# Kernel tuning notes

Measured on AMD Instinct MI355X. Metric: run time of the kernel, lower is better.

## Reference

```python
import jax, jax.numpy as jnp
import numpy as np

CAPACITY_FACTOR = 1.25


def setup_inputs() -> dict:
    key = jax.random.key(0)
    ks = jax.random.split(key, 5)
    B, N, D, E, H = 4, 2048, 1024, 8, 4096
    x = jax.random.normal(ks[0], (B, N, D), dtype=jnp.float32)
    w_router = jax.random.normal(ks[1], (D, E), dtype=jnp.float32) * 0.02
    w1 = jax.random.normal(ks[2], (E, D, H), dtype=jnp.float32) * 0.02
    b1 = jnp.zeros((E, H), dtype=jnp.float32)
    w2 = jax.random.normal(ks[3], (E, H, D), dtype=jnp.float32) * 0.02
    b2 = jnp.zeros((E, D), dtype=jnp.float32)
    return {"x": x, "w_router": w_router, "w1": w1, "b1": b1, "w2": w2, "b2": b2}


def reference(x, w_router, w1, b1, w2, b2):
    B, N, D = x.shape
    E = w_router.shape[1]
    C = int(N * CAPACITY_FACTOR // E)  # expert capacity

    # ---- top-1 switch router ----
    logits = jnp.einsum('bnd,de->bne', x, w_router)                 # [B,N,E]
    z = jax.nn.logsumexp(logits, axis=-1)                           # [B,N]
    router_z_loss = jnp.mean(z * z)
    probs = jax.nn.softmax(logits, axis=-1)                         # [B,N,E]
    gate = jnp.max(probs, axis=-1)                                  # [B,N]
    idx = jnp.argmax(probs, axis=-1)                                # [B,N]
    mask = jax.nn.one_hot(idx, E, dtype=x.dtype)                    # [B,N,E]

    # load-balancing aux loss (Switch-Transformer style)
    density = jnp.mean(mask, axis=1)                                # [B,E] fraction routed
    density_proxy = jnp.mean(probs, axis=1)                         # [B,E] mean router prob
    aux_loss = jnp.mean(jnp.sum(density * density_proxy, axis=-1)) * (E * E)

    # position within each expert; drop tokens beyond capacity
    pos = jnp.cumsum(mask, axis=1) - 1.0                            # [B,N,E]
    pos = pos.astype(jnp.int32)
    # one_hot zeros out indices outside [0,C); mask zeros unrouted slots
    dispatch = mask[..., None] * jax.nn.one_hot(pos, C, dtype=x.dtype)  # [B,N,E,C]
    combine = dispatch * gate[:, :, None, None]                     # [B,N,E,C]

    # ---- dense dispatch -> grouped expert FFN -> dense combine ----
    expert_inputs = jnp.einsum('bnd,bnec->becd', x, dispatch)       # [B,E,C,D]
    h = jax.nn.gelu(jnp.einsum('becd,edh->bech', expert_inputs, w1)
                    + b1[None, :, None, :])                          # [B,E,C,H]
    expert_outputs = jnp.einsum('bech,ehd->becd', h, w2) + b2[None, :, None, :]
    output = jnp.einsum('becd,bnec->bnd', expert_outputs, combine)  # [B,N,D]
    return output, aux_loss, router_z_loss
```

## Files before the change

kernel.cpp:

```cpp
#include <hip/hip_runtime.h>
#include <hip/hip_bf16.h>
#include <math.h>

#define B_ 4
#define N_ 2048
#define D_ 1024
#define E_ 8
#define H_ 4096
#define C_ 320
#define M_ (B_*C_)

typedef __attribute__((ext_vector_type(8))) short short8;
typedef __attribute__((ext_vector_type(4))) float floatx4;

__device__ __forceinline__ unsigned short f2bf(float f) {
  unsigned u = __builtin_bit_cast(unsigned, f);
  u += 0x7fffu + ((u >> 16) & 1u);
  return (unsigned short)(u >> 16);
}

__device__ __forceinline__ float gelu_fast(float x) {
  float u = 0.7978845608028654f * (x + 0.044715f * x * x * x);
  float t = 1.f - 2.f / (__expf(2.f * u) + 1.f);
  return 0.5f * x * (1.f + t);
}

__device__ __forceinline__ void gload_lds16(const unsigned short* g, unsigned short* l) {
  __builtin_amdgcn_global_load_lds(
      (const __attribute__((address_space(1))) unsigned int*)g,
      (__attribute__((address_space(3))) unsigned int*)l, 16, 0, 0);
}

__global__ __launch_bounds__(256) void router_kernel(
    const float* __restrict__ x, const float* __restrict__ wr,
    int* __restrict__ idx_buf, float* __restrict__ gate_buf,
    float* __restrict__ stats)
{
  int lane  = threadIdx.x & 63;
  int wave  = threadIdx.x >> 6;
  int token = blockIdx.x * 4 + wave;
  int b     = token >> 11;

  const float* xp = x + (size_t)token * D_ + lane * 16;
  float xv[16];
#pragma unroll
  for (int i = 0; i < 4; i++) {
    float4 v = ((const float4*)xp)[i];
    xv[i*4+0]=v.x; xv[i*4+1]=v.y; xv[i*4+2]=v.z; xv[i*4+3]=v.w;
  }
  double acc[8];
#pragma unroll
  for (int e = 0; e < 8; e++) acc[e] = 0.0;
  const float* wp = wr + (size_t)(lane * 16) * E_;
#pragma unroll
  for (int i = 0; i < 16; i++) {
    float xs = xv[i];
#pragma unroll
    for (int e = 0; e < 8; e++) acc[e] += (double)xs * (double)wp[i*8 + e];
  }
  for (int off = 32; off > 0; off >>= 1) {
#pragma unroll
    for (int e = 0; e < 8; e++) acc[e] += __shfl_xor(acc[e], off, 64);
  }

  float l[8];
#pragma unroll
  for (int e = 0; e < 8; e++) l[e] = (float)acc[e];
  float m = l[0]; int best = 0;
#pragma unroll
  for (int e = 1; e < 8; e++) if (l[e] > m) { m = l[e]; best = e; }
  float p[8], sum = 0.f;
#pragma unroll
  for (int e = 0; e < 8; e++) { p[e] = expf(l[e] - m); sum += p[e]; }
  float inv = 1.f / sum;
#pragma unroll
  for (int e = 0; e < 8; e++) p[e] *= inv;
  float z    = m + logf(sum);
  float gate = inv;

  __shared__ float s_cnt[8], s_prox[8], s_zsq[1];
  if (threadIdx.x < 8)  { s_cnt[threadIdx.x] = 0.f; s_prox[threadIdx.x] = 0.f; }
  if (threadIdx.x == 8) s_zsq[0] = 0.f;
  __syncthreads();
  if (lane == 0) {
    idx_buf[token]  = best;
    gate_buf[token] = gate;
    atomicAdd(&s_zsq[0], z * z);
    atomicAdd(&s_cnt[best], 1.f);
#pragma unroll
    for (int e = 0; e < 8; e++) atomicAdd(&s_prox[e], p[e]);
  }
  __syncthreads();
  if (threadIdx.x < 8) {
    atomicAdd(&stats[b*8 + threadIdx.x],      s_cnt[threadIdx.x]);
    atomicAdd(&stats[32 + b*8 + threadIdx.x], s_prox[threadIdx.x]);
  }
  if (threadIdx.x == 8) atomicAdd(&stats[64], s_zsq[0]);
}

__global__ __launch_bounds__(64) void pos_kernel(
    const int* __restrict__ idx_buf, int* __restrict__ slot_token,
    const float* __restrict__ stats, float* __restrict__ loss_out)
{
  int be = blockIdx.x;
  int b = be >> 3, e = be & 7;
  int lane = threadIdx.x;
  int base = 0;
  int* out = slot_token + (size_t)(e * B_ + b) * C_;
  for (int n0 = 0; n0 < N_; n0 += 64) {
    int n = n0 + lane;
    bool match = (idx_buf[b * N_ + n] == e);
    unsigned long long mask = __ballot(match);
    int my = base + __popcll(mask & ((1ull << lane) - 1ull));
    if (match && my < C_) out[my] = b * N_ + n;
    base += __popcll(mask);
  }
  if (be == 0 && lane == 0) {
    float aux = 0.f;
    for (int i = 0; i < 32; i++) aux += stats[i] * stats[32 + i];
    aux *= 64.f / ((float)B_ * (float)N_ * (float)N_);
    loss_out[0] = aux;
    loss_out[1] = stats[64] / (float)(B_ * N_);
  }
}

__global__ __launch_bounds__(256) void gather_kernel(
    const float* __restrict__ x, const int* __restrict__ slot_token,
    unsigned short* __restrict__ xe)
{
  int row = blockIdx.x;
  int t = slot_token[row];
  int col = threadIdx.x * 4;
  ushort4 o;
  if (t >= 0) {
    float4 v = *(const float4*)(x + (size_t)t * D_ + col);
    o.x = f2bf(v.x); o.y = f2bf(v.y); o.z = f2bf(v.z); o.w = f2bf(v.w);
  } else {
    o.x = 0; o.y = 0; o.z = 0; o.w = 0;
  }
  *(ushort4*)(xe + (size_t)row * D_ + col) = o;
}

__global__ __launch_bounds__(256) void transcast_kernel(
    const float* __restrict__ in, unsigned short* __restrict__ out, int R, int Cc)
{
  int e = blockIdx.z;
  const float* pin = in + (size_t)e * R * Cc;
  unsigned short* pout = out + (size_t)e * R * Cc;
  __shared__ float T[64][65];
  int r0 = blockIdx.y * 64, c0 = blockIdx.x * 64;
  {
    int row = threadIdx.x >> 2;
    int cb  = (threadIdx.x & 3) * 4;
#pragma unroll
    for (int p = 0; p < 4; p++) {
      int col = cb + p * 16;
      float4 v = *(const float4*)(pin + (size_t)(r0 + row) * Cc + c0 + col);
      T[row][col+0] = v.x; T[row][col+1] = v.y; T[row][col+2] = v.z; T[row][col+3] = v.w;
    }
  }
  __syncthreads();
  {
    int ocb = threadIdx.x >> 4;
    int or4 = (threadIdx.x & 15) * 4;
#pragma unroll
    for (int p = 0; p < 4; p++) {
      int oc = ocb + p * 16;
      ushort4 o;
      o.x = f2bf(T[or4+0][oc]); o.y = f2bf(T[or4+1][oc]);
      o.z = f2bf(T[or4+2][oc]); o.w = f2bf(T[or4+3][oc]);
      *(ushort4*)(pout + (size_t)(c0 + oc) * R + r0 + or4) = o;
    }
  }
}

template<int EPI>
__global__ __launch_bounds__(256) void gemm_kernel(
    const unsigned short* __restrict__ A,
    const unsigned short* __restrict__ BT,
    const float* __restrict__ bias,
    unsigned short* __restrict__ Hout,
    float* __restrict__ Out,
    const int* __restrict__ slot_token,
    const float* __restrict__ gate_buf,
    int M, int K, int Nn, int MT)
{
  int e  = blockIdx.x & 7;
  int s  = blockIdx.x >> 3;
  int m0 = (s % MT) * 128;
  int n0 = (s / MT) * 128;
  const unsigned short* Ae = A  + (size_t)e * M  * K;
  const unsigned short* Be = BT + (size_t)e * Nn * K;

  __shared__ __align__(16) unsigned short As[2][128 * 32];
  __shared__ __align__(16) unsigned short Bs[2][128 * 32];
  __shared__ int   s_tok[128];
  __shared__ float s_gate[128];

  int tid  = threadIdx.x;
  int lane = tid & 63;
  int wave = tid >> 6;
  int wm   = (wave >> 1) * 64;
  int wn   = (wave & 1) * 64;
  int lr   = lane & 15;
  int quad = lane >> 4;

  if constexpr (EPI == 1) {
    if (tid < 128) {
      int t = slot_token[(size_t)e * M + m0 + tid];
      s_tok[tid]  = t;
      s_gate[tid] = (t >= 0) ? gate_buf[t] : 0.f;
    }
  }

  floatx4 acc[4][4];
#pragma unroll
  for (int i = 0; i < 4; i++)
#pragma unroll
    for (int j = 0; j < 4; j++) acc[i][j] = (floatx4){0.f, 0.f, 0.f, 0.f};

  int rA0 = wave * 32 + (lane >> 2);
  int kcc = (lane & 3) * 8;
  const unsigned short* Ag0 = Ae + (size_t)(m0 + rA0)      * K + kcc;
  const unsigned short* Ag1 = Ae + (size_t)(m0 + rA0 + 16) * K + kcc;
  const unsigned short* Bg0 = Be + (size_t)(n0 + rA0)      * K + kcc;
  const unsigned short* Bg1 = Be + (size_t)(n0 + rA0 + 16) * K + kcc;
  const unsigned offA0 = (wave * 32) * 32;
  const unsigned offA1 = (wave * 32 + 16) * 32;

  gload_lds16(Ag0, &As[0][offA0]);
  gload_lds16(Ag1, &As[0][offA1]);
  gload_lds16(Bg0, &Bs[0][offA0]);
  gload_lds16(Bg1, &Bs[0][offA1]);
  Ag0 += 32; Ag1 += 32; Bg0 += 32; Bg1 += 32;

  int nIter = K >> 5;
  int buf = 0;
  for (int it = 0; it < nIter; ++it) {
    __syncthreads();
    if (it + 1 < nIter) {
      gload_lds16(Ag0, &As[buf ^ 1][offA0]);
      gload_lds16(Ag1, &As[buf ^ 1][offA1]);
      gload_lds16(Bg0, &Bs[buf ^ 1][offA0]);
      gload_lds16(Bg1, &Bs[buf ^ 1][offA1]);
      Ag0 += 32; Ag1 += 32; Bg0 += 32; Bg1 += 32;
    }
    short8 af[4], bf[4];
#pragma unroll
    for (int i = 0; i < 4; i++) {
      af[i] = *(const short8*)(&As[buf][(wm + i * 16 + lr) * 32 + quad * 8]);
      bf[i] = *(const short8*)(&Bs[buf][(wn + i * 16 + lr) * 32 + quad * 8]);
    }
#pragma unroll
    for (int i = 0; i < 4; i++)
#pragma unroll
      for (int j = 0; j < 4; j++)
        acc[i][j] = __builtin_amdgcn_mfma_f32_16x16x32_bf16(af[i], bf[j], acc[i][j], 0, 0, 0);
    buf ^= 1;
  }

#pragma unroll
  for (int i = 0; i < 4; i++) {
    int rloc = wm + i * 16 + quad * 4;
#pragma unroll
    for (int j = 0; j < 4; j++) {
      int col = n0 + wn + j * 16 + lr;
      float bz = bias[(size_t)e * Nn + col];
      if constexpr (EPI == 0) {
        size_t base = (size_t)e * M * Nn + (size_t)(m0 + rloc) * Nn + col;
#pragma unroll
        for (int r = 0; r < 4; r++)
          Hout[base + (size_t)r * Nn] = f2bf(gelu_fast(acc[i][j][r] + bz));
      } else {
#pragma unroll
        for (int r = 0; r < 4; r++) {
          int t = s_tok[rloc + r];
          if (t >= 0)
            Out[(size_t)t * D_ + col] = s_gate[rloc + r] * (acc[i][j][r] + bz);
        }
      }
    }
  }
}

extern "C" void kernel_launch(void* const* d_in, const int* in_sizes, int n_in,
                              void* d_out, int out_size, void* d_ws, size_t ws_size,
                              hipStream_t stream)
{
  (void)in_sizes; (void)n_in; (void)ws_size;
  const float* x  = (const float*)d_in[0];
  const float* wr = (const float*)d_in[1];
  const float* w1 = (const float*)d_in[2];
  const float* b1 = (const float*)d_in[3];
  const float* w2 = (const float*)d_in[4];
  const float* b2 = (const float*)d_in[5];
  float* out = (float*)d_out;

  char* ws = (char*)d_ws;
  int*   idx_buf  = (int*)(ws + 0);
  float* gate_buf = (float*)(ws + 32768);
  float* stats    = (float*)(ws + 65536);
  int*   slot_tok = (int*)(ws + 66560);
  unsigned short* xe  = (unsigned short*)(ws + 107520);
  unsigned short* wbf = (unsigned short*)(ws + 21079040);
  unsigned short* hbf = (unsigned short*)(ws + 88187904);

  hipMemsetAsync(d_out, 0, (size_t)out_size * 4, stream);
  hipMemsetAsync(stats, 0, 1024, stream);
  hipMemsetAsync(slot_tok, 0xFF, (size_t)E_ * B_ * C_ * 4, stream);

  router_kernel<<<(B_ * N_) / 4, 256, 0, stream>>>(x, wr, idx_buf, gate_buf, stats);
  pos_kernel<<<B_ * E_, 64, 0, stream>>>(idx_buf, slot_tok, stats,
                                         out + (size_t)B_ * N_ * D_);
  gather_kernel<<<E_ * M_, 256, 0, stream>>>(x, slot_tok, xe);

  transcast_kernel<<<dim3(H_ / 64, D_ / 64, E_), 256, 0, stream>>>(w1, wbf, D_, H_);
  gemm_kernel<0><<<E_ * (H_ / 128) * (M_ / 128), 256, 0, stream>>>(
      xe, wbf, b1, hbf, nullptr, nullptr, nullptr, M_, D_, H_, M_ / 128);
  transcast_kernel<<<dim3(D_ / 64, H_ / 64, E_), 256, 0, stream>>>(w2, wbf, H_, D_);
  gemm_kernel<1><<<E_ * (D_ / 128) * (M_ / 128), 256, 0, stream>>>(
      hbf, wbf, b2, nullptr, out, slot_tok, gate_buf, M_, H_, D_, M_ / 128);
}
```

Baseline: 644.6 us.

## Enlarge expert GEMM tiles to 256x256x64 with swizzled LDS and interleaved prefetch

The grouped expert GEMMs move from 128x128 tiles with K-step 32 and 4 waves to 256x256 tiles with K-step 64 and 8 waves. Each wave now computes a 128x64 sub-tile, and the LDS layout uses an XOR swizzle to avoid bank conflicts. The main loop is split into four MFMA phases, with explicit barriers, wave-priority hints and staged global-to-LDS prefetches of the next A and B slices. The aim is more data reuse per load and better overlap of loads with MFMA work. The trade-off is 128KB of LDS per block, which allows only one block per CU, and far fewer blocks: the second GEMM gets only 160 blocks, which may leave many of the GPU's CUs idle.

```diff
diff --git a/kernel.cpp b/kernel.cpp
--- a/kernel.cpp
+++ b/kernel.cpp
@@ -175,7 +175,7 @@
 }
 
 template<int EPI>
-__global__ __launch_bounds__(256) void gemm_kernel(
+__global__ __launch_bounds__(512, 2) void gemm_kernel(
     const unsigned short* __restrict__ A,
     const unsigned short* __restrict__ BT,
     const float* __restrict__ bias,
@@ -187,96 +187,188 @@
 {
   int e  = blockIdx.x & 7;
   int s  = blockIdx.x >> 3;
-  int m0 = (s % MT) * 128;
-  int n0 = (s / MT) * 128;
+  int m0 = (s % MT) * 256;
+  int n0 = (s / MT) * 256;
   const unsigned short* Ae = A  + (size_t)e * M  * K;
   const unsigned short* Be = BT + (size_t)e * Nn * K;
 
-  __shared__ __align__(16) unsigned short As[2][128 * 32];
-  __shared__ __align__(16) unsigned short Bs[2][128 * 32];
-  __shared__ int   s_tok[128];
-  __shared__ float s_gate[128];
+  __shared__ __align__(16) unsigned short As[2][256 * 64];
+  __shared__ __align__(16) unsigned short Bs[2][256 * 64];
+  __shared__ int   s_tok[256];
+  __shared__ float s_gate[256];
 
   int tid  = threadIdx.x;
   int lane = tid & 63;
-  int wave = tid >> 6;
-  int wm   = (wave >> 1) * 64;
-  int wn   = (wave & 1) * 64;
+  int w    = tid >> 6;
+  int wm   = (w >> 2) * 128;
+  int wn   = (w & 3) * 64;
   int lr   = lane & 15;
   int quad = lane >> 4;
+  int c0 = (((quad    ) ^ (lane & 7)) << 3);
+  int c1 = (((quad + 4) ^ (lane & 7)) << 3);
 
   if constexpr (EPI == 1) {
-    if (tid < 128) {
+    if (tid < 256) {
       int t = slot_token[(size_t)e * M + m0 + tid];
       s_tok[tid]  = t;
       s_gate[tid] = (t >= 0) ? gate_buf[t] : 0.f;
     }
   }
 
-  floatx4 acc[4][4];
-#pragma unroll
-  for (int i = 0; i < 4; i++)
+  floatx4 acc[8][4];
+#pragma unroll
+  for (int i = 0; i < 8; i++)
 #pragma unroll
     for (int j = 0; j < 4; j++) acc[i][j] = (floatx4){0.f, 0.f, 0.f, 0.f};
 
-  int rA0 = wave * 32 + (lane >> 2);
-  int kcc = (lane & 3) * 8;
-  const unsigned short* Ag0 = Ae + (size_t)(m0 + rA0)      * K + kcc;
-  const unsigned short* Ag1 = Ae + (size_t)(m0 + rA0 + 16) * K + kcc;
-  const unsigned short* Bg0 = Be + (size_t)(n0 + rA0)      * K + kcc;
-  const unsigned short* Bg1 = Be + (size_t)(n0 + rA0 + 16) * K + kcc;
-  const unsigned offA0 = (wave * 32) * 32;
-  const unsigned offA1 = (wave * 32 + 16) * 32;
-
-  gload_lds16(Ag0, &As[0][offA0]);
-  gload_lds16(Ag1, &As[0][offA1]);
-  gload_lds16(Bg0, &Bs[0][offA0]);
-  gload_lds16(Bg1, &Bs[0][offA1]);
-  Ag0 += 32; Ag1 += 32; Bg0 += 32; Bg1 += 32;
-
-  int nIter = K >> 5;
-  int buf = 0;
-  for (int it = 0; it < nIter; ++it) {
-    __syncthreads();
-    if (it + 1 < nIter) {
-      gload_lds16(Ag0, &As[buf ^ 1][offA0]);
-      gload_lds16(Ag1, &As[buf ^ 1][offA1]);
-      gload_lds16(Bg0, &Bs[buf ^ 1][offA0]);
-      gload_lds16(Bg1, &Bs[buf ^ 1][offA1]);
-      Ag0 += 32; Ag1 += 32; Bg0 += 32; Bg1 += 32;
-    }
-    short8 af[4], bf[4];
-#pragma unroll
-    for (int i = 0; i < 4; i++) {
-      af[i] = *(const short8*)(&As[buf][(wm + i * 16 + lr) * 32 + quad * 8]);
-      bf[i] = *(const short8*)(&Bs[buf][(wn + i * 16 + lr) * 32 + quad * 8]);
-    }
-#pragma unroll
-    for (int i = 0; i < 4; i++)
-#pragma unroll
-      for (int j = 0; j < 4; j++)
-        acc[i][j] = __builtin_amdgcn_mfma_f32_16x16x32_bf16(af[i], bf[j], acc[i][j], 0, 0, 0);
-    buf ^= 1;
-  }
-
-#pragma unroll
-  for (int i = 0; i < 4; i++) {
-    int rloc = wm + i * 16 + quad * 4;
-#pragma unroll
-    for (int j = 0; j < 4; j++) {
-      int col = n0 + wn + j * 16 + lr;
+  int rrow = lane >> 3;
+  int sch  = ((lane & 7) ^ rrow) << 3;
+  const unsigned short* gA00 = Ae + (size_t)(m0       + w*16     + rrow) * K + sch;
+  const unsigned short* gA01 = Ae + (size_t)(m0       + w*16 + 8 + rrow) * K + sch;
+  const unsigned short* gA10 = Ae + (size_t)(m0 + 128 + w*16     + rrow) * K + sch;
+  const unsigned short* gA11 = Ae + (size_t)(m0 + 128 + w*16 + 8 + rrow) * K + sch;
+  const unsigned short* gB00 = Be + (size_t)(n0       + w*16     + rrow) * K + sch;
+  const unsigned short* gB01 = Be + (size_t)(n0       + w*16 + 8 + rrow) * K + sch;
+  const unsigned short* gB10 = Be + (size_t)(n0 + 128 + w*16     + rrow) * K + sch;
+  const unsigned short* gB11 = Be + (size_t)(n0 + 128 + w*16 + 8 + rrow) * K + sch;
+
+#define STAGE_A0(dbuf) do { \
+    gload_lds16(gA00, &As[dbuf][(w*16    ) * 64]); \
+    gload_lds16(gA01, &As[dbuf][(w*16 + 8) * 64]); \
+    gA00 += 64; gA01 += 64; } while (0)
+#define STAGE_A1(dbuf) do { \
+    gload_lds16(gA10, &As[dbuf][(128 + w*16    ) * 64]); \
+    gload_lds16(gA11, &As[dbuf][(128 + w*16 + 8) * 64]); \
+    gA10 += 64; gA11 += 64; } while (0)
+#define STAGE_B0(dbuf) do { \
+    gload_lds16(gB00, &Bs[dbuf][(w*16    ) * 64]); \
+    gload_lds16(gB01, &Bs[dbuf][(w*16 + 8) * 64]); \
+    gB00 += 64; gB01 += 64; } while (0)
+#define STAGE_B1(dbuf) do { \
+    gload_lds16(gB10, &Bs[dbuf][(128 + w*16    ) * 64]); \
+    gload_lds16(gB11, &Bs[dbuf][(128 + w*16 + 8) * 64]); \
+    gB10 += 64; gB11 += 64; } while (0)
+
+  int nt = K >> 6;
+  STAGE_A0(0); STAGE_A1(0); STAGE_B0(0); STAGE_B1(0);
+  if (nt > 1) {
+    STAGE_A0(1); STAGE_A1(1);
+    asm volatile("s_waitcnt vmcnt(4)" ::: "memory");
+  } else {
+    asm volatile("s_waitcnt vmcnt(0)" ::: "memory");
+  }
+  __builtin_amdgcn_s_barrier();
+
+  short8 af[4][2], bf[4][2];
+  int cur = 0;
+  for (int t = 0; t < nt; ++t) {
+    int nxt = cur ^ 1;
+#pragma unroll
+    for (int m = 0; m < 4; ++m) {
+      int row = wm + m * 16 + lr;
+      af[m][0] = *(const short8*)&As[cur][row * 64 + c0];
+      af[m][1] = *(const short8*)&As[cur][row * 64 + c1];
+    }
+#pragma unroll
+    for (int n = 0; n < 2; ++n) {
+      int row = wn + n * 16 + lr;
+      bf[n][0] = *(const short8*)&Bs[cur][row * 64 + c0];
+      bf[n][1] = *(const short8*)&Bs[cur][row * 64 + c1];
+    }
+    if (t + 1 < nt) STAGE_B0(nxt);
+    __builtin_amdgcn_s_barrier();
+    asm volatile("s_waitcnt lgkmcnt(0)" ::: "memory");
+    __builtin_amdgcn_sched_barrier(0);
+    __builtin_amdgcn_s_setprio(1);
+#pragma unroll
+    for (int m = 0; m < 4; ++m)
+#pragma unroll
+      for (int n = 0; n < 2; ++n) {
+        acc[m][n] = __builtin_amdgcn_mfma_f32_16x16x32_bf16(af[m][0], bf[n][0], acc[m][n], 0, 0, 0);
+        acc[m][n] = __builtin_amdgcn_mfma_f32_16x16x32_bf16(af[m][1], bf[n][1], acc[m][n], 0, 0, 0);
+      }
+    __builtin_amdgcn_s_setprio(0);
+    __builtin_amdgcn_s_barrier();
+#pragma unroll
+    for (int n = 0; n < 2; ++n) {
+      int row = wn + (n + 2) * 16 + lr;
+      bf[n+2][0] = *(const short8*)&Bs[cur][row * 64 + c0];
+      bf[n+2][1] = *(const short8*)&Bs[cur][row * 64 + c1];
+    }
+    if (t + 1 < nt) STAGE_B1(nxt);
+    __builtin_amdgcn_s_barrier();
+    asm volatile("s_waitcnt lgkmcnt(0)" ::: "memory");
+    __builtin_amdgcn_sched_barrier(0);
+    __builtin_amdgcn_s_setprio(1);
+#pragma unroll
+    for (int m = 0; m < 4; ++m)
+#pragma unroll
+      for (int n = 2; n < 4; ++n) {
+        acc[m][n] = __builtin_amdgcn_mfma_f32_16x16x32_bf16(af[m][0], bf[n][0], acc[m][n], 0, 0, 0);
+        acc[m][n] = __builtin_amdgcn_mfma_f32_16x16x32_bf16(af[m][1], bf[n][1], acc[m][n], 0, 0, 0);
+      }
+    __builtin_amdgcn_s_setprio(0);
+    __builtin_amdgcn_s_barrier();
+#pragma unroll
+    for (int m = 0; m < 4; ++m) {
+      int row = wm + 64 + m * 16 + lr;
+      af[m][0] = *(const short8*)&As[cur][row * 64 + c0];
+      af[m][1] = *(const short8*)&As[cur][row * 64 + c1];
+    }
+    __builtin_amdgcn_s_barrier();
+    asm volatile("s_waitcnt lgkmcnt(0)" ::: "memory");
+    __builtin_amdgcn_sched_barrier(0);
+    __builtin_amdgcn_s_setprio(1);
+#pragma unroll
+    for (int m = 0; m < 4; ++m)
+#pragma unroll
+      for (int n = 2; n < 4; ++n) {
+        acc[m+4][n] = __builtin_amdgcn_mfma_f32_16x16x32_bf16(af[m][0], bf[n][0], acc[m+4][n], 0, 0, 0);
+        acc[m+4][n] = __builtin_amdgcn_mfma_f32_16x16x32_bf16(af[m][1], bf[n][1], acc[m+4][n], 0, 0, 0);
+      }
+    __builtin_amdgcn_s_setprio(0);
+    __builtin_amdgcn_s_barrier();
+    if (t + 2 < nt) { STAGE_A0(cur); STAGE_A1(cur); }
+    __builtin_amdgcn_s_barrier();
+    __builtin_amdgcn_s_setprio(1);
+#pragma unroll
+    for (int m = 0; m < 4; ++m)
+#pragma unroll
+      for (int n = 0; n < 2; ++n) {
+        acc[m+4][n] = __builtin_amdgcn_mfma_f32_16x16x32_bf16(af[m][0], bf[n][0], acc[m+4][n], 0, 0, 0);
+        acc[m+4][n] = __builtin_amdgcn_mfma_f32_16x16x32_bf16(af[m][1], bf[n][1], acc[m+4][n], 0, 0, 0);
+      }
+    __builtin_amdgcn_s_setprio(0);
+    if (t + 1 < nt) {
+      if (t + 2 < nt) asm volatile("s_waitcnt vmcnt(4)" ::: "memory");
+      else            asm volatile("s_waitcnt vmcnt(0)" ::: "memory");
+    }
+    __builtin_amdgcn_s_barrier();
+    cur = nxt;
+  }
+#undef STAGE_A0
+#undef STAGE_A1
+#undef STAGE_B0
+#undef STAGE_B1
+
+#pragma unroll
+  for (int m = 0; m < 8; ++m) {
+    int rloc = wm + m * 16 + quad * 4;
+#pragma unroll
+    for (int n = 0; n < 4; ++n) {
+      int col = n0 + wn + n * 16 + lr;
       float bz = bias[(size_t)e * Nn + col];
       if constexpr (EPI == 0) {
         size_t base = (size_t)e * M * Nn + (size_t)(m0 + rloc) * Nn + col;
 #pragma unroll
         for (int r = 0; r < 4; r++)
-          Hout[base + (size_t)r * Nn] = f2bf(gelu_fast(acc[i][j][r] + bz));
+          Hout[base + (size_t)r * Nn] = f2bf(gelu_fast(acc[m][n][r] + bz));
       } else {
 #pragma unroll
         for (int r = 0; r < 4; r++) {
           int t = s_tok[rloc + r];
           if (t >= 0)
-            Out[(size_t)t * D_ + col] = s_gate[rloc + r] * (acc[i][j][r] + bz);
+            Out[(size_t)t * D_ + col] = s_gate[rloc + r] * (acc[m][n][r] + bz);
         }
       }
     }
@@ -315,9 +407,9 @@
   gather_kernel<<<E_ * M_, 256, 0, stream>>>(x, slot_tok, xe);
 
   transcast_kernel<<<dim3(H_ / 64, D_ / 64, E_), 256, 0, stream>>>(w1, wbf, D_, H_);
-  gemm_kernel<0><<<E_ * (H_ / 128) * (M_ / 128), 256, 0, stream>>>(
-      xe, wbf, b1, hbf, nullptr, nullptr, nullptr, M_, D_, H_, M_ / 128);
+  gemm_kernel<0><<<E_ * (H_ / 256) * (M_ / 256), 512, 0, stream>>>(
+      xe, wbf, b1, hbf, nullptr, nullptr, nullptr, M_, D_, H_, M_ / 256);
   transcast_kernel<<<dim3(D_ / 64, H_ / 64, E_), 256, 0, stream>>>(w2, wbf, H_, D_);
-  gemm_kernel<1><<<E_ * (D_ / 128) * (M_ / 128), 256, 0, stream>>>(
-      hbf, wbf, b2, nullptr, out, slot_tok, gate_buf, M_, H_, D_, M_ / 128);
-}
+  gemm_kernel<1><<<E_ * (D_ / 256) * (M_ / 256), 512, 0, stream>>>(
+      hbf, wbf, b2, nullptr, out, slot_tok, gate_buf, M_, H_, D_, M_ / 256);
+}
```

Measured after the change: 665.3 us. 3.2% more time.

## Swizzle LDS tiles, add explicit waitcnt/barrier pipeline and occupancy hint in GEMM

Applied to the files above, without the earlier changes.

Rewrites the GEMM main loop so global-to-LDS loads use an XOR-swizzled column chunk, and the fragment reads apply the matching swizzle. The goal is to avoid LDS bank conflicts on the short8 reads. The plain __syncthreads is replaced with explicit vmcnt/lgkmcnt waits, raw s_barrier, sched_barrier and setprio around the MFMA block, and launch_bounds now requests 4 blocks per CU. The intent is better overlap and less stalling, at the risk of register pressure under the occupancy cap and a full vmcnt(0) wait each iteration.

```diff
diff --git a/kernel.cpp b/kernel.cpp
--- a/kernel.cpp
+++ b/kernel.cpp
@@ -175,7 +175,7 @@
 }
 
 template<int EPI>
-__global__ __launch_bounds__(256) void gemm_kernel(
+__global__ __launch_bounds__(256, 4) void gemm_kernel(
     const unsigned short* __restrict__ A,
     const unsigned short* __restrict__ BT,
     const float* __restrict__ bias,
@@ -199,11 +199,12 @@
 
   int tid  = threadIdx.x;
   int lane = tid & 63;
-  int wave = tid >> 6;
-  int wm   = (wave >> 1) * 64;
-  int wn   = (wave & 1) * 64;
+  int w    = tid >> 6;
+  int wm   = (w >> 1) * 64;
+  int wn   = (w & 1) * 64;
   int lr   = lane & 15;
   int quad = lane >> 4;
+  int rch  = ((quad ^ ((lr >> 1) & 3)) << 3);
 
   if constexpr (EPI == 1) {
     if (tid < 128) {
@@ -219,64 +220,71 @@
 #pragma unroll
     for (int j = 0; j < 4; j++) acc[i][j] = (floatx4){0.f, 0.f, 0.f, 0.f};
 
-  int rA0 = wave * 32 + (lane >> 2);
-  int kcc = (lane & 3) * 8;
-  const unsigned short* Ag0 = Ae + (size_t)(m0 + rA0)      * K + kcc;
-  const unsigned short* Ag1 = Ae + (size_t)(m0 + rA0 + 16) * K + kcc;
-  const unsigned short* Bg0 = Be + (size_t)(n0 + rA0)      * K + kcc;
-  const unsigned short* Bg1 = Be + (size_t)(n0 + rA0 + 16) * K + kcc;
-  const unsigned offA0 = (wave * 32) * 32;
-  const unsigned offA1 = (wave * 32 + 16) * 32;
-
-  gload_lds16(Ag0, &As[0][offA0]);
-  gload_lds16(Ag1, &As[0][offA1]);
-  gload_lds16(Bg0, &Bs[0][offA0]);
-  gload_lds16(Bg1, &Bs[0][offA1]);
-  Ag0 += 32; Ag1 += 32; Bg0 += 32; Bg1 += 32;
-
-  int nIter = K >> 5;
-  int buf = 0;
-  for (int it = 0; it < nIter; ++it) {
-    __syncthreads();
-    if (it + 1 < nIter) {
-      gload_lds16(Ag0, &As[buf ^ 1][offA0]);
-      gload_lds16(Ag1, &As[buf ^ 1][offA1]);
-      gload_lds16(Bg0, &Bs[buf ^ 1][offA0]);
-      gload_lds16(Bg1, &Bs[buf ^ 1][offA1]);
-      Ag0 += 32; Ag1 += 32; Bg0 += 32; Bg1 += 32;
-    }
-    short8 af[4], bf[4];
-#pragma unroll
-    for (int i = 0; i < 4; i++) {
-      af[i] = *(const short8*)(&As[buf][(wm + i * 16 + lr) * 32 + quad * 8]);
-      bf[i] = *(const short8*)(&Bs[buf][(wn + i * 16 + lr) * 32 + quad * 8]);
-    }
-#pragma unroll
-    for (int i = 0; i < 4; i++)
-#pragma unroll
-      for (int j = 0; j < 4; j++)
-        acc[i][j] = __builtin_amdgcn_mfma_f32_16x16x32_bf16(af[i], bf[j], acc[i][j], 0, 0, 0);
-    buf ^= 1;
-  }
-
-#pragma unroll
-  for (int i = 0; i < 4; i++) {
-    int rloc = wm + i * 16 + quad * 4;
-#pragma unroll
-    for (int j = 0; j < 4; j++) {
-      int col = n0 + wn + j * 16 + lr;
+  unsigned kA   = (unsigned)K * 2;
+  unsigned soff = (unsigned)((lane & 3) ^ ((lane >> 3) & 3)) * 16u
+                + (unsigned)(lane >> 2) * kA;
+  unsigned aoff = (unsigned)(m0 + w * 16) * kA + soff;
+  unsigned boff = (unsigned)(n0 + w * 16) * kA + soff;
+  const char* AeC = (const char*)Ae;
+  const char* BeC = (const char*)Be;
+
+#define STAGE_A(dbuf) do { \
+    gload_lds16((const unsigned short*)(AeC + aoff),           &As[dbuf][(w * 16) * 32]); \
+    gload_lds16((const unsigned short*)(AeC + aoff + 64 * kA), &As[dbuf][(64 + w * 16) * 32]); \
+    aoff += 64; } while (0)
+#define STAGE_B(dbuf) do { \
+    gload_lds16((const unsigned short*)(BeC + boff),           &Bs[dbuf][(w * 16) * 32]); \
+    gload_lds16((const unsigned short*)(BeC + boff + 64 * kA), &Bs[dbuf][(64 + w * 16) * 32]); \
+    boff += 64; } while (0)
+
+  int nt = K >> 5;
+  STAGE_A(0); STAGE_B(0);
+  asm volatile("s_waitcnt vmcnt(0)" ::: "memory");
+  __builtin_amdgcn_s_barrier();
+
+  for (int t = 0; t < nt; ++t) {
+    int cur = t & 1, nxt = cur ^ 1;
+    if (t + 1 < nt) { STAGE_A(nxt); STAGE_B(nxt); }
+    short8 a[4], b[4];
+#pragma unroll
+    for (int m = 0; m < 4; ++m)
+      a[m] = *(const short8*)&As[cur][(wm + m * 16 + lr) * 32 + rch];
+#pragma unroll
+    for (int n = 0; n < 4; ++n)
+      b[n] = *(const short8*)&Bs[cur][(wn + n * 16 + lr) * 32 + rch];
+    asm volatile("s_waitcnt lgkmcnt(0)" ::: "memory");
+    __builtin_amdgcn_sched_barrier(0);
+    __builtin_amdgcn_s_setprio(1);
+#pragma unroll
+    for (int m = 0; m < 4; ++m)
+#pragma unroll
+      for (int n = 0; n < 4; ++n)
+        acc[m][n] = __builtin_amdgcn_mfma_f32_16x16x32_bf16(a[m], b[n], acc[m][n], 0, 0, 0);
+    __builtin_amdgcn_s_setprio(0);
+    if (t + 1 < nt) asm volatile("s_waitcnt vmcnt(0)" ::: "memory");
+    __builtin_amdgcn_s_barrier();
+  }
+#undef STAGE_A
+#undef STAGE_B
+
+#pragma unroll
+  for (int m = 0; m < 4; ++m) {
+    int rloc = wm + m * 16 + quad * 4;
+#pragma unroll
+    for (int n = 0; n < 4; ++n) {
+      int col = n0 + wn + n * 16 + lr;
       float bz = bias[(size_t)e * Nn + col];
       if constexpr (EPI == 0) {
         size_t base = (size_t)e * M * Nn + (size_t)(m0 + rloc) * Nn + col;
 #pragma unroll
         for (int r = 0; r < 4; r++)
-          Hout[base + (size_t)r * Nn] = f2bf(gelu_fast(acc[i][j][r] + bz));
+          Hout[base + (size_t)r * Nn] = f2bf(gelu_fast(acc[m][n][r] + bz));
       } else {
 #pragma unroll
         for (int r = 0; r < 4; r++) {
           int t = s_tok[rloc + r];
           if (t >= 0)
-            Out[(size_t)t * D_ + col] = s_gate[rloc + r] * (acc[i][j][r] + bz);
+            Out[(size_t)t * D_ + col] = s_gate[rloc + r] * (acc[m][n][r] + bz);
         }
       }
     }
```

After: 621.9 us. 1.04x faster.
